# Kernel optimization log

Hardware: AMD Instinct MI355X
Metric: run time of the kernel (lower is better)

The kernel has to match this reference:

```python
import jax, jax.numpy as jnp
import numpy as np

ALPHA = 0.2          # LeakyReLU negative slope
NEG_INF = -9e15      # mask value used by the original module


def setup_inputs() -> dict:
    key = jax.random.key(0)
    k1, k2, k3, k4 = jax.random.split(key, 4)
    N, Din, Dout = 8192, 512, 256
    features = jax.random.normal(k1, (N, Din), dtype=jnp.float32)
    adj = jax.random.randint(k2, (N, N), 0, 2, dtype=jnp.int32)
    W = jax.random.normal(k3, (Din, Dout), dtype=jnp.float32) * (1.414 / np.sqrt(Din))
    a = jax.random.normal(k4, (2 * Dout, 1), dtype=jnp.float32) * (1.414 / np.sqrt(2 * Dout))
    return {"features": features, "adj": adj, "W": W, "a": a}


def reference(features, adj, W, a):
    Dout = W.shape[1]
    Wh = features @ W                       # [N, Dout]
    # e_ij = leakyrelu([Wh_i || Wh_j] @ a) decomposes additively:
    # identical math to the N*N*2D concat in the original, without materializing it.
    src = Wh @ a[:Dout, 0]                  # [N]  contribution of node i
    dst = Wh @ a[Dout:, 0]                  # [N]  contribution of node j
    e = jax.nn.leaky_relu(src[:, None] + dst[None, :], negative_slope=ALPHA)  # [N, N]
    masked = jnp.where(adj > 0, e, NEG_INF)
    attention = jax.nn.softmax(masked, axis=1)   # dropout p=0.0 (eval) -> identity
    h_prime = attention @ Wh                # [N, Dout]
    return jax.nn.elu(h_prime)
```

## Files before the change

### kernel.cpp

```cpp
#include <hip/hip_runtime.h>
#include <hip/hip_bf16.h>

#define NN   8192
#define DIN  512
#define DOUT 256

typedef __attribute__((ext_vector_type(8)))  short s16x8;
typedef __attribute__((ext_vector_type(16))) float f32x16;

static __device__ __forceinline__ unsigned short f2bf(float f) {
    union { float f; unsigned u; } v; v.f = f;
    unsigned r = v.u + 0x7fffu + ((v.u >> 16) & 1u);
    return (unsigned short)(r >> 16);
}

static __device__ __forceinline__ void gload_lds16(const void* g, void* l) {
    __builtin_amdgcn_global_load_lds(
        (const __attribute__((address_space(1))) unsigned int*)g,
        (__attribute__((address_space(3))) unsigned int*)l, 16, 0, 0);
}

__global__ __launch_bounds__(256) void k_wh2(const float* __restrict__ feat,
                                             const float* __restrict__ W,
                                             const float* __restrict__ a,
                                             unsigned short* __restrict__ WhT,
                                             float* __restrict__ src,
                                             float* __restrict__ dst) {
    __shared__ float lf[16 * DIN];
    __shared__ float red[2][4][16];
    const int tid = threadIdx.x;
    const int i0  = blockIdx.x * 16;
    const int w   = tid >> 6, lane = tid & 63;

    const float4* fsrc = (const float4*)(feat + (size_t)i0 * DIN);
    float4* fdst = (float4*)lf;
    #pragma unroll
    for (int q = 0; q < 8; ++q) fdst[tid + q * 256] = fsrc[tid + q * 256];
    __syncthreads();

    const int c = tid;
    float outs[16];
    #pragma unroll
    for (int r = 0; r < 16; ++r) outs[r] = 0.f;

    for (int k = 0; k < DIN; k += 4) {
        float w0 = W[(k + 0) * DOUT + c];
        float w1 = W[(k + 1) * DOUT + c];
        float w2 = W[(k + 2) * DOUT + c];
        float w3 = W[(k + 3) * DOUT + c];
        #pragma unroll
        for (int r = 0; r < 16; ++r) {
            float4 f = *(const float4*)&lf[r * DIN + k];
            outs[r] = fmaf(f.x, w0, fmaf(f.y, w1, fmaf(f.z, w2, fmaf(f.w, w3, outs[r]))));
        }
    }

    unsigned short tb[16];
    #pragma unroll
    for (int r = 0; r < 16; ++r) tb[r] = f2bf(outs[r]);
    uint4* wt = (uint4*)(WhT + (size_t)c * NN + i0);
    wt[0] = *(uint4*)&tb[0];
    wt[1] = *(uint4*)&tb[8];

    const float as_ = a[c], ad_ = a[DOUT + c];
    #pragma unroll
    for (int r = 0; r < 16; ++r) {
        float s = outs[r] * as_;
        float d = outs[r] * ad_;
        #pragma unroll
        for (int off = 32; off; off >>= 1) {
            s += __shfl_xor(s, off);
            d += __shfl_xor(d, off);
        }
        if (lane == 0) { red[0][w][r] = s; red[1][w][r] = d; }
    }
    __syncthreads();
    if (tid < 16)
        src[i0 + tid] = red[0][0][tid] + red[0][1][tid] + red[0][2][tid] + red[0][3][tid];
    else if (tid < 32) {
        int r = tid - 16;
        dst[i0 + r] = red[1][0][r] + red[1][1][r] + red[1][2][r] + red[1][3][r];
    }
}

__global__ __launch_bounds__(256) void k_mask(const int* __restrict__ adj,
                                              unsigned char* __restrict__ bits) {
    const int gid = blockIdx.x * 256 + threadIdx.x;
    const int kb  = gid & 7;
    const int tq  = (gid >> 3) & 7;
    const int s_  = (gid >> 6) & 3;
    const int row = gid >> 8;
    const int* base = adj + ((size_t)row * NN + s_ * 2048 + tq * 256 + kb * 8);

    int4 v[8];
    #pragma unroll
    for (int j = 0; j < 4; ++j) {
        v[2 * j]     = *(const int4*)(base + j * 64);
        v[2 * j + 1] = *(const int4*)(base + j * 64 + 4);
    }
    unsigned int u = 0;
    #pragma unroll
    for (int j = 0; j < 4; ++j) {
        unsigned int m = (v[2*j].x   > 0 ? 1u   : 0u) | (v[2*j].y   > 0 ? 2u   : 0u) |
                         (v[2*j].z   > 0 ? 4u   : 0u) | (v[2*j].w   > 0 ? 8u   : 0u) |
                         (v[2*j+1].x > 0 ? 16u  : 0u) | (v[2*j+1].y > 0 ? 32u  : 0u) |
                         (v[2*j+1].z > 0 ? 64u  : 0u) | (v[2*j+1].w > 0 ? 128u : 0u);
        u |= m << (8 * j);
    }
    *(unsigned int*)(bits + (size_t)row * 1024 + s_ * 256 + kb * 32 + tq * 4) = u;
}

#define STEP5(T, CUR)                                                                    \
{                                                                                        \
    {                   \
        const int tn_ = ((T) < 31) ? (T) + 1 : 31;                                       \
        const size_t gkb_ = (size_t)(kb0 + tn_ * 64) * 2;                                \
        _Pragma("unroll")                                                                \
        for (int q = 0; q < 4; ++q)                                                      \
            gload_lds16((const char*)WhT + (size_t)colB[q] * (NN * 2) + gkb_ + kbB[q],   \
                        Bs[(CUR) ^ 1] + (q * 512 + tid) * 16);                           \
    }                                                                                    \
                                                     \
    _Pragma("unroll")                                                                    \
    for (int ks4 = 0; ks4 < 4; ++ks4) {                                                  \
        const int kbyte_ = ks4 * 32 + lhi * 16;                                          \
        const int colg_  = c0w + l31;                                                    \
        s16x8 bfv_ = *(const s16x8*)(Bs[CUR] + colg_ * 128 +                             \
                                     (kbyte_ ^ ((colg_ & 7) << 4)));                     \
        _Pragma("unroll")                                                                \
        for (int mt = 0; mt < 2; ++mt) {                                                 \
            const int row_ = mt * 32 + l31;                                              \
            s16x8 afv_ = *(const s16x8*)(Pl[CUR] + row_ * 128 +                          \
                                         (kbyte_ ^ ((row_ & 7) << 4)));                  \
            acc[mt] = __builtin_amdgcn_mfma_f32_32x32x16_bf16(afv_, bfv_, acc[mt], 0, 0, 0); \
        }                                                                                \
    }                                                                                    \
    if ((T) < 31) {                                       \
        const unsigned int m8_ = browp[(T) + 1];                                         \
        float4 d0_ = *(const float4*)(dstp + ((T) + 1) * 64);                            \
        float4 d1_ = *(const float4*)(dstp + ((T) + 1) * 64 + 4);                        \
        const float dd_[8] = {d0_.x, d0_.y, d0_.z, d0_.w, d1_.x, d1_.y, d1_.z, d1_.w};   \
        s16x8 pw_;                                                                       \
        _Pragma("unroll")                                                                \
        for (int jj = 0; jj < 8; ++jj) {                                                 \
            float x_ = si + dd_[jj];                                                     \
            x_ = fmaxf(x_, 0.2f * x_);                               \
            float p_ = (m8_ >> jj) & 1u ? __expf(x_) : 0.f;     \
            den += p_;                                                                   \
            pw_[jj] = (short)f2bf(p_);                                                   \
        }                                                                                \
        *(s16x8*)(Pl[(CUR) ^ 1] + pbyte) = pw_;                                          \
    }                                                                                    \
    asm volatile("s_waitcnt vmcnt(0) lgkmcnt(0)" ::: "memory");                          \
    __builtin_amdgcn_s_barrier();                                                        \
}

__global__ __launch_bounds__(512, 4) void k_attn5(const unsigned char* __restrict__ bits,
                                                  const unsigned short* __restrict__ WhT,
                                                  const float* __restrict__ src,
                                                  const float* __restrict__ dstg,
                                                  float* __restrict__ denp,
                                                  float* __restrict__ part) {
    __shared__ __attribute__((aligned(16))) char Bs[2][32768];
    __shared__ __attribute__((aligned(16))) char Pl[2][8192];

    const int tid  = threadIdx.x;
    const int lane = tid & 63;
    const int w    = tid >> 6;
    const int l31  = lane & 31, lhi = lane >> 5;
    const int c0w  = w * 32;

    const int rt  = blockIdx.x & 127;
    const int ks  = blockIdx.x >> 7;
    const int kb0 = ks * 2048;

    const int r  = tid >> 3, kb = tid & 7;
    const int gr = rt * 64 + r;
    const float si = src[gr];
    const unsigned char* browp = bits + (size_t)gr * 1024 + ks * 256 + kb * 32;
    const float* dstp = dstg + kb0 + kb * 8;
    const int pbyte = r * 128 + ((kb * 16) ^ ((r & 7) << 4));

    int colB[4], kbB[4];
    #pragma unroll
    for (int q = 0; q < 4; ++q) {
        int chunk = q * 512 + tid;
        colB[q] = chunk >> 3;
        kbB[q]  = ((chunk & 7) * 16) ^ ((colB[q] & 7) << 4);
    }

    f32x16 acc[2];
    #pragma unroll
    for (int mt = 0; mt < 2; ++mt)
        #pragma unroll
        for (int e = 0; e < 16; ++e) acc[mt][e] = 0.f;
    float den = 0.f;

    #pragma unroll
    for (int q = 0; q < 4; ++q)
        gload_lds16((const char*)WhT + (size_t)colB[q] * (NN * 2) + (size_t)kb0 * 2 + kbB[q],
                    Bs[0] + (q * 512 + tid) * 16);
    {
        const unsigned int m8 = browp[0];
        float4 d0 = *(const float4*)(dstp);
        float4 d1 = *(const float4*)(dstp + 4);
        const float dd[8] = {d0.x, d0.y, d0.z, d0.w, d1.x, d1.y, d1.z, d1.w};
        s16x8 pw;
        #pragma unroll
        for (int jj = 0; jj < 8; ++jj) {
            float x = si + dd[jj];
            x = fmaxf(x, 0.2f * x);
            float p = (m8 >> jj) & 1u ? __expf(x) : 0.f;
            den += p;
            pw[jj] = (short)f2bf(p);
        }
        *(s16x8*)(Pl[0] + pbyte) = pw;
    }
    asm volatile("s_waitcnt vmcnt(0) lgkmcnt(0)" ::: "memory");
    __builtin_amdgcn_s_barrier();

    for (int tt = 0; tt < 16; ++tt) {
        STEP5(2 * tt,     0);
        STEP5(2 * tt + 1, 1);
    }

    den += __shfl_xor(den, 1);
    den += __shfl_xor(den, 2);
    den += __shfl_xor(den, 4);
    if ((tid & 7) == 0) denp[(size_t)ks * NN + gr] = den;

    float* pp = part + (size_t)ks * (NN * DOUT);
    #pragma unroll
    for (int mt = 0; mt < 2; ++mt) {
        #pragma unroll
        for (int e = 0; e < 16; ++e) {
            const int row = rt * 64 + mt * 32 + (e & 3) + 8 * (e >> 2) + 4 * lhi;
            pp[(size_t)row * DOUT + c0w + l31] = acc[mt][e];
        }
    }
}

__global__ __launch_bounds__(256) void k_finish2(const float* __restrict__ part,
                                                 const float* __restrict__ denp,
                                                 float* __restrict__ out) {
    const int idx = blockIdx.x * 256 + threadIdx.x;
    const int row = idx >> 6;
    float den = denp[row] + denp[NN + row] + denp[2 * NN + row] + denp[3 * NN + row];
    float rv = den > 0.f ? 1.f / den : 0.f;
    const int st = NN * DOUT / 4;
    const float4* p = (const float4*)part;
    float4 va = p[idx], vb = p[idx + st], vc = p[idx + 2 * st], vd = p[idx + 3 * st];
    float4 s;
    s.x = (va.x + vb.x + vc.x + vd.x) * rv;
    s.y = (va.y + vb.y + vc.y + vd.y) * rv;
    s.z = (va.z + vb.z + vc.z + vd.z) * rv;
    s.w = (va.w + vb.w + vc.w + vd.w) * rv;
    s.x = s.x > 0.f ? s.x : expm1f(s.x);
    s.y = s.y > 0.f ? s.y : expm1f(s.y);
    s.z = s.z > 0.f ? s.z : expm1f(s.z);
    s.w = s.w > 0.f ? s.w : expm1f(s.w);
    ((float4*)out)[idx] = s;
}

extern "C" void kernel_launch(void* const* d_in, const int* in_sizes, int n_in,
                              void* d_out, int out_size, void* d_ws, size_t ws_size,
                              hipStream_t stream) {
    const float* feat = (const float*)d_in[0];
    const int*   adj  = (const int*)d_in[1];
    const float* W    = (const float*)d_in[2];
    const float* a    = (const float*)d_in[3];
    float* out = (float*)d_out;

    char* ws = (char*)d_ws;
    unsigned short* WhT  = (unsigned short*)ws;
    float*          src  = (float*)(ws + 4194304);
    float*          dst  = (float*)(ws + 4227072);
    float*          denp = (float*)(ws + 4259840);
    unsigned char*  bits = (unsigned char*)(ws + 4390912);
    float*          part = (float*)(ws + 12779520);

    k_mask   <<<8192, 256, 0, stream>>>(adj, bits);
    k_wh2    <<<512,  256, 0, stream>>>(feat, W, a, WhT, src, dst);
    k_attn5  <<<512,  512, 0, stream>>>(bits, WhT, src, dst, denp, part);
    k_finish2<<<2048, 256, 0, stream>>>(part, denp, out);
}
```

Baseline: 193.5 us.

## Load WhT B-fragments directly to registers and simplify mask bit layout

The attention kernel stops staging WhT tiles in LDS through async global-to-LDS copies. Each lane now loads its MFMA B fragments straight from global memory into registers, which frees 64KB of LDS per block and removes the double-buffered B pipeline. The mask kernel is rewritten so each block packs one row with contiguous 32-element chunks per thread, and the attention kernel's bit indexing is changed to match. The trade-off is that global loads now sit on the MFMA critical path with no explicit prefetch, and duplicate loads across waves may go to L2.

```diff
diff --git a/kernel.cpp b/kernel.cpp
--- a/kernel.cpp
+++ b/kernel.cpp
@@ -12,12 +12,6 @@
     union { float f; unsigned u; } v; v.f = f;
     unsigned r = v.u + 0x7fffu + ((v.u >> 16) & 1u);
     return (unsigned short)(r >> 16);
-}
-
-static __device__ __forceinline__ void gload_lds16(const void* g, void* l) {
-    __builtin_amdgcn_global_load_lds(
-        (const __attribute__((address_space(1))) unsigned int*)g,
-        (__attribute__((address_space(3))) unsigned int*)l, 16, 0, 0);
 }
 
 __global__ __launch_bounds__(256) void k_wh2(const float* __restrict__ feat,
@@ -85,58 +79,31 @@
 
 __global__ __launch_bounds__(256) void k_mask(const int* __restrict__ adj,
                                               unsigned char* __restrict__ bits) {
-    const int gid = blockIdx.x * 256 + threadIdx.x;
-    const int kb  = gid & 7;
-    const int tq  = (gid >> 3) & 7;
-    const int s_  = (gid >> 6) & 3;
-    const int row = gid >> 8;
-    const int* base = adj + ((size_t)row * NN + s_ * 2048 + tq * 256 + kb * 8);
-
-    int4 v[8];
-    #pragma unroll
-    for (int j = 0; j < 4; ++j) {
-        v[2 * j]     = *(const int4*)(base + j * 64);
-        v[2 * j + 1] = *(const int4*)(base + j * 64 + 4);
-    }
+    const int row = blockIdx.x;
+    const int tid = threadIdx.x;
+    const int* base = adj + (size_t)row * NN + tid * 32;
     unsigned int u = 0;
     #pragma unroll
-    for (int j = 0; j < 4; ++j) {
-        unsigned int m = (v[2*j].x   > 0 ? 1u   : 0u) | (v[2*j].y   > 0 ? 2u   : 0u) |
-                         (v[2*j].z   > 0 ? 4u   : 0u) | (v[2*j].w   > 0 ? 8u   : 0u) |
-                         (v[2*j+1].x > 0 ? 16u  : 0u) | (v[2*j+1].y > 0 ? 32u  : 0u) |
-                         (v[2*j+1].z > 0 ? 64u  : 0u) | (v[2*j+1].w > 0 ? 128u : 0u);
-        u |= m << (8 * j);
-    }
-    *(unsigned int*)(bits + (size_t)row * 1024 + s_ * 256 + kb * 32 + tq * 4) = u;
-}
-
-#define STEP5(T, CUR)                                                                    \
+    for (int j = 0; j < 8; ++j) {
+        int4 v = *(const int4*)(base + j * 4);
+        unsigned int b = (v.x > 0 ? 1u : 0u) | (v.y > 0 ? 2u : 0u) |
+                         (v.z > 0 ? 4u : 0u) | (v.w > 0 ? 8u : 0u);
+        u |= b << (j * 4);
+    }
+    *(unsigned int*)(bits + (size_t)row * 1024 + tid * 4) = u;
+}
+
+
+#define STEP6(T, CUR)                                                                    \
 {                                                                                        \
-    {                   \
-        const int tn_ = ((T) < 31) ? (T) + 1 : 31;                                       \
-        const size_t gkb_ = (size_t)(kb0 + tn_ * 64) * 2;                                \
-        _Pragma("unroll")                                                                \
-        for (int q = 0; q < 4; ++q)                                                      \
-            gload_lds16((const char*)WhT + (size_t)colB[q] * (NN * 2) + gkb_ + kbB[q],   \
-                        Bs[(CUR) ^ 1] + (q * 512 + tid) * 16);                           \
-    }                                                                                    \
-                                                     \
+        \
+    s16x8 bfr_[4];                                                                       \
     _Pragma("unroll")                                                                    \
-    for (int ks4 = 0; ks4 < 4; ++ks4) {                                                  \
-        const int kbyte_ = ks4 * 32 + lhi * 16;                                          \
-        const int colg_  = c0w + l31;                                                    \
-        s16x8 bfv_ = *(const s16x8*)(Bs[CUR] + colg_ * 128 +                             \
-                                     (kbyte_ ^ ((colg_ & 7) << 4)));                     \
-        _Pragma("unroll")                                                                \
-        for (int mt = 0; mt < 2; ++mt) {                                                 \
-            const int row_ = mt * 32 + l31;                                              \
-            s16x8 afv_ = *(const s16x8*)(Pl[CUR] + row_ * 128 +                          \
-                                         (kbyte_ ^ ((row_ & 7) << 4)));                  \
-            acc[mt] = __builtin_amdgcn_mfma_f32_32x32x16_bf16(afv_, bfv_, acc[mt], 0, 0, 0); \
-        }                                                                                \
-    }                                                                                    \
-    if ((T) < 31) {                                       \
-        const unsigned int m8_ = browp[(T) + 1];                                         \
+    for (int ks4 = 0; ks4 < 4; ++ks4)                                                    \
+        bfr_[ks4] = *(const s16x8*)(WhTb + (T) * 64 + ks4 * 16);                         \
+                                       \
+    if ((T) < 31) {                                                                      \
+        const unsigned int m8_ = browp[((T) + 1) * 8];                                   \
         float4 d0_ = *(const float4*)(dstp + ((T) + 1) * 64);                            \
         float4 d1_ = *(const float4*)(dstp + ((T) + 1) * 64 + 4);                        \
         const float dd_[8] = {d0_.x, d0_.y, d0_.z, d0_.w, d1_.x, d1_.y, d1_.z, d1_.w};   \
@@ -151,17 +118,27 @@
         }                                                                                \
         *(s16x8*)(Pl[(CUR) ^ 1] + pbyte) = pw_;                                          \
     }                                                                                    \
-    asm volatile("s_waitcnt vmcnt(0) lgkmcnt(0)" ::: "memory");                          \
-    __builtin_amdgcn_s_barrier();                                                        \
-}
-
-__global__ __launch_bounds__(512, 4) void k_attn5(const unsigned char* __restrict__ bits,
+                             \
+    _Pragma("unroll")                                                                    \
+    for (int ks4 = 0; ks4 < 4; ++ks4) {                                                  \
+        const int kbyte_ = ks4 * 32 + lhi * 16;                                          \
+        _Pragma("unroll")                                                                \
+        for (int mt = 0; mt < 2; ++mt) {                                                 \
+            const int row_ = mt * 32 + l31;                                              \
+            s16x8 afv_ = *(const s16x8*)(Pl[CUR] + row_ * 128 +                          \
+                                         (kbyte_ ^ ((row_ & 7) << 4)));                  \
+            acc[mt] = __builtin_amdgcn_mfma_f32_32x32x16_bf16(afv_, bfr_[ks4], acc[mt], 0, 0, 0); \
+        }                                                                                \
+    }                                                                                    \
+    __syncthreads();                \
+}
+
+__global__ __launch_bounds__(512, 4) void k_attn6(const unsigned char* __restrict__ bits,
                                                   const unsigned short* __restrict__ WhT,
                                                   const float* __restrict__ src,
                                                   const float* __restrict__ dstg,
                                                   float* __restrict__ denp,
                                                   float* __restrict__ part) {
-    __shared__ __attribute__((aligned(16))) char Bs[2][32768];
     __shared__ __attribute__((aligned(16))) char Pl[2][8192];
 
     const int tid  = threadIdx.x;
@@ -174,21 +151,15 @@
     const int ks  = blockIdx.x >> 7;
     const int kb0 = ks * 2048;
 
+    const unsigned short* WhTb = WhT + (size_t)(c0w + l31) * NN + kb0 + lhi * 8;
+
     const int r  = tid >> 3, kb = tid & 7;
     const int gr = rt * 64 + r;
     const float si = src[gr];
-    const unsigned char* browp = bits + (size_t)gr * 1024 + ks * 256 + kb * 32;
+    const unsigned char* browp = bits + (size_t)gr * 1024 + ks * 256 + kb;
     const float* dstp = dstg + kb0 + kb * 8;
     const int pbyte = r * 128 + ((kb * 16) ^ ((r & 7) << 4));
 
-    int colB[4], kbB[4];
-    #pragma unroll
-    for (int q = 0; q < 4; ++q) {
-        int chunk = q * 512 + tid;
-        colB[q] = chunk >> 3;
-        kbB[q]  = ((chunk & 7) * 16) ^ ((colB[q] & 7) << 4);
-    }
-
     f32x16 acc[2];
     #pragma unroll
     for (int mt = 0; mt < 2; ++mt)
@@ -196,10 +167,6 @@
         for (int e = 0; e < 16; ++e) acc[mt][e] = 0.f;
     float den = 0.f;
 
-    #pragma unroll
-    for (int q = 0; q < 4; ++q)
-        gload_lds16((const char*)WhT + (size_t)colB[q] * (NN * 2) + (size_t)kb0 * 2 + kbB[q],
-                    Bs[0] + (q * 512 + tid) * 16);
     {
         const unsigned int m8 = browp[0];
         float4 d0 = *(const float4*)(dstp);
@@ -216,12 +183,11 @@
         }
         *(s16x8*)(Pl[0] + pbyte) = pw;
     }
-    asm volatile("s_waitcnt vmcnt(0) lgkmcnt(0)" ::: "memory");
-    __builtin_amdgcn_s_barrier();
+    __syncthreads();
 
     for (int tt = 0; tt < 16; ++tt) {
-        STEP5(2 * tt,     0);
-        STEP5(2 * tt + 1, 1);
+        STEP6(2 * tt,     0);
+        STEP6(2 * tt + 1, 1);
     }
 
     den += __shfl_xor(den, 1);
@@ -281,6 +247,6 @@
 
     k_mask   <<<8192, 256, 0, stream>>>(adj, bits);
     k_wh2    <<<512,  256, 0, stream>>>(feat, W, a, WhT, src, dst);
-    k_attn5  <<<512,  512, 0, stream>>>(bits, WhT, src, dst, denp, part);
+    k_attn6  <<<512,  512, 0, stream>>>(bits, WhT, src, dst, denp, part);
     k_finish2<<<2048, 256, 0, stream>>>(part, denp, out);
 }
```

Result: slower. 212.1 us (+9.6%).
